# Performance work log

Hardware: AMD Instinct MI355X
Metric: run time of the kernel (lower is better)

## Reference

```python
import jax, jax.numpy as jnp
import numpy as np

COMMITMENT_COST = 0.25

def setup_inputs() -> dict:
    key = jax.random.key(0)
    k1, k2 = jax.random.split(key)
    z = jax.random.normal(k1, (32768, 512), dtype=jnp.float32)
    # codebook initialized uniform(-1/K, 1/K) as in the torch module
    K = 8192
    W = jax.random.uniform(k2, (K, 512), dtype=jnp.float32, minval=-1.0 / K, maxval=1.0 / K)
    return {"z": z, "W": W}

def reference(z, W):
    # z: [B, D], W: [K, D]
    # squared-distance expansion: ||z||^2 + ||w||^2 - 2 z.w
    d2 = (jnp.sum(z * z, axis=1, keepdims=True)
          + jnp.sum(W * W, axis=1)
          - 2.0 * jnp.einsum('bd,kd->bk', z, W))  # [B, K]
    indices = jnp.argmin(d2, axis=1)              # [B]
    z_q_raw = W[indices]                          # [B, D]
    e_latent_loss = jnp.mean((jax.lax.stop_gradient(z_q_raw) - z) ** 2)
    q_latent_loss = jnp.mean((z_q_raw - jax.lax.stop_gradient(z)) ** 2)
    vq_loss = q_latent_loss + COMMITMENT_COST * e_latent_loss
    # straight-through estimator
    z_q = z + jax.lax.stop_gradient(z_q_raw - z)
    return (z_q, indices, vq_loss)
```

## Files before the change

kernel.cpp:

```cpp
#include <hip/hip_runtime.h>
#include <stdint.h>


#define B_ROWS 32768
#define DIM    512
#define KCODES 8192
#define SUPERS 4
#define TILES  16
#define ZROWS  64

typedef short bhalf8_t __attribute__((ext_vector_type(8)));
typedef float f32x4_t  __attribute__((ext_vector_type(4)));

__device__ __forceinline__ float b2f(unsigned short u) {
    return __uint_as_float(((unsigned int)u) << 16);
}
__device__ __forceinline__ unsigned short f2b(float f) {
    unsigned int x = __float_as_uint(f);
    return (unsigned short)((x + 0x7FFFu + ((x >> 16) & 1u)) >> 16);
}
__device__ __forceinline__ void gl_lds16(const void* g, void* l) {
    __builtin_amdgcn_global_load_lds(
        (const __attribute__((address_space(1))) unsigned int*)g,
        (__attribute__((address_space(3))) unsigned int*)l, 16, 0, 0);
}

__global__ __launch_bounds__(256) void k_split(const float4* __restrict__ src,
                                               ushort4* __restrict__ dst, int n4) {
    int i = blockIdx.x * 256 + threadIdx.x;
    int stride = gridDim.x * 256;
    for (; i < n4; i += stride) {
        float4 v = src[i];
        ushort4 h;
        h.x = f2b(v.x); h.y = f2b(v.y); h.z = f2b(v.z); h.w = f2b(v.w);
        dst[i] = h;
    }
}

__global__ __launch_bounds__(256) void k_pairsq(const float* __restrict__ X,
                                                float* __restrict__ out, int nrows) {
    int wid = threadIdx.x >> 6, lane = threadIdx.x & 63;
    int r = blockIdx.x * 4 + wid;
    if (r >= nrows) return;
    int b = lane >> 3, j = lane & 7;
    float acc = 0.f;
    if (b < 4) {
        const float* x = X + (size_t)r * DIM + b * 128 + j;
        float v = x[0];
        acc = __fmul_rn(v, v);
        for (int i = 1; i < 16; i++) {
            float w = x[8 * i];
            acc = __fadd_rn(acc, __fmul_rn(w, w));
        }
    }
    float t = __fadd_rn(acc, __shfl_xor(acc, 1));
    t = __fadd_rn(t, __shfl_xor(t, 2));
    t = __fadd_rn(t, __shfl_xor(t, 4));
    float u = __fadd_rn(t, __shfl_xor(t, 8));
    u = __fadd_rn(u, __shfl_xor(u, 16));
    if (lane == 0) out[r] = u;
}

__global__ __launch_bounds__(256) void k_argmin(const unsigned short* __restrict__ Zh,
                                                const unsigned short* __restrict__ Wh,
                                                const float* __restrict__ ww,
                                                float2* __restrict__ part) {
    __shared__ alignas(16) unsigned char smem[73728];
    const int tid = threadIdx.x;
    const int lane = tid & 63, w = tid >> 6;
    const int wm = w >> 1, wn = w & 1;
    const int lane15 = lane & 15, q = lane >> 4;
    const int b = blockIdx.x;
    const int super = b & 3;
    const int rb = (b >> 2) * ZROWS;

    unsigned char* zl = smem;
    unsigned char* wl = smem + 65536;

    {
        const int m = tid & 15;
        const int kseg8 = ((tid >> 4) & 3) << 3;
#pragma unroll
        for (int i = 0; i < 16; i++) {
            const int s = i * 256 + tid;
            const int ks = s >> 8;
            const int g = (s >> 6) & 3;
            gl_lds16(Zh + (size_t)(rb + g * 16 + m) * DIM + ks * 32 + kseg8,
                     zl + s * 16);
        }
    }

    const int rowO0 = ((tid >> 6) << 4) | (tid & 15);
    const int kO0   = ((tid >> 4) & 3) << 3;
    const int dst0  = tid * 16;

    uint32_t p1[2][4], p2[2][4];
#pragma unroll
    for (int i = 0; i < 2; i++)
#pragma unroll
        for (int jj = 0; jj < 4; jj++) { p1[i][jj] = 0xFFFFFFFFu; p2[i][jj] = 0xFFFFFFFFu; }

    __syncthreads();

    for (int tl = 0; tl < TILES; ++tl) {
        const int nt = super * 2048 + tl * 128;
        f32x4_t acc[2][4];
#pragma unroll
        for (int i = 0; i < 2; i++)
#pragma unroll
            for (int jj = 0; jj < 4; jj++) acc[i][jj] = (f32x4_t){0.f, 0.f, 0.f, 0.f};

        for (int ks = 0; ks < 16; ++ks) {
            __syncthreads();
            const int kg = ks * 32 + kO0;
            gl_lds16(Wh + (size_t)(nt + rowO0) * DIM + kg,      wl + dst0);
            gl_lds16(Wh + (size_t)(nt + rowO0 + 64) * DIM + kg, wl + 4096 + dst0);
            __syncthreads();

            bhalf8_t af[2], bf[4];
#pragma unroll
            for (int f = 0; f < 2; f++)
                af[f] = *(const bhalf8_t*)(zl + ks * 4096 + (wm * 2 + f) * 1024 + lane * 16);
#pragma unroll
            for (int f = 0; f < 4; f++)
                bf[f] = *(const bhalf8_t*)(wl + (wn * 4096 + f * 1024) + lane * 16);
#pragma unroll
            for (int fm = 0; fm < 2; fm++)
#pragma unroll
                for (int fn = 0; fn < 4; fn++)
                    acc[fm][fn] = __builtin_amdgcn_mfma_f32_16x16x32_bf16(af[fm], bf[fn], acc[fm][fn], 0, 0, 0);
        }

        float cb[4];
#pragma unroll
        for (int fn = 0; fn < 4; fn++)
            cb[fn] = ww[nt + wn * 64 + fn * 16 + lane15] + 0.5f;
#pragma unroll
        for (int fm = 0; fm < 2; fm++)
#pragma unroll
            for (int r = 0; r < 4; r++)
#pragma unroll
                for (int fn = 0; fn < 4; fn++) {
                    float sv = fmaf(-2.0f, acc[fm][fn][r], cb[fn]);
                    uint32_t pk = (__float_as_uint(sv) & 0xFFFFFF80u) | (uint32_t)(tl * 4 + fn);
                    if (pk < p1[fm][r]) { p2[fm][r] = p1[fm][r]; p1[fm][r] = pk; }
                    else if (pk < p2[fm][r]) { p2[fm][r] = pk; }
                }
    }

    __syncthreads();
    uint32_t* keys = (uint32_t*)smem;
#pragma unroll
    for (int fm = 0; fm < 2; fm++)
#pragma unroll
        for (int r = 0; r < 4; r++) {
            int row = wm * 32 + fm * 16 + q * 4 + r;
            int slice = wn * 16 + lane15;
            keys[(row * 32 + slice) * 2 + 0] = p1[fm][r];
            keys[(row * 32 + slice) * 2 + 1] = p2[fm][r];
        }
    __syncthreads();
    if (tid < ZROWS) {
        int row = tid;
        int rglob = rb + row;
        for (int s = 0; s < 4; s++) {
            uint32_t bk = 0xFFFFFFFFu; int be = 0;
            for (int e = 0; e < 64; e++) {
                uint32_t k = keys[row * 64 + e];
                if (k < bk) { bk = k; be = e; }
            }
            int slice = be >> 1;
            int id = (int)(bk & 127u);
            int n = super * 2048 + (id >> 2) * 128 + (slice >> 4) * 64 + (id & 3) * 16 + (slice & 15);
            part[((size_t)rglob * SUPERS + super) * 4 + s] =
                make_float2(__uint_as_float(bk), __int_as_float(n));
            keys[row * 64 + be] = 0xFFFFFFFFu;
        }
    }
}

__global__ __launch_bounds__(256) void k_exact(const float* __restrict__ Zf,
                                               const float* __restrict__ Wf,
                                               const float2* __restrict__ part,
                                               const float* __restrict__ zz,
                                               const float* __restrict__ ww,
                                               float* __restrict__ outf,
                                               float* __restrict__ lossp) {
    __shared__ float wsum[4];
    int wid = threadIdx.x >> 6, lane = threadIdx.x & 63;
    int r = blockIdx.x * 4 + wid;
    int c = lane >> 2, j = lane & 3;

    float2 P = part[((size_t)r * SUPERS + (c >> 2)) * 4 + (c & 3)];
    int n = __float_as_int(P.y);
    n = min(max(n, 0), KCODES - 1);

    const float* zp = Zf + (size_t)r * DIM + j;
    const float* wp = Wf + (size_t)n * DIM + j;
    float acc = 0.f;
    for (int i = 0; i < 128; i++)
        acc = __fadd_rn(acc, __fmul_rn(zp[4 * i], wp[4 * i]));
    float t = __fadd_rn(acc, __shfl_xor(acc, 1));
    t = __fadd_rn(t, __shfl_xor(t, 2));
    float dot = __shfl(t, c * 4);

    float t1 = __fadd_rn(zz[r], ww[n]);
    float t2 = __fmul_rn(2.0f, dot);
    float d2 = __fadd_rn(t1, -t2);

    float bd = (j == 0) ? d2 : 3.4e38f;
    int   bn = (j == 0) ? n  : 0x7FFFFFFF;
#pragma unroll
    for (int off = 32; off; off >>= 1) {
        float od = __shfl_xor(bd, off);
        int   on = __shfl_xor(bn, off);
        if (od < bd || (od == bd && on < bn)) { bd = od; bn = on; }
    }
    int idx = bn;

    float4 wa = *(const float4*)(Wf + (size_t)idx * DIM + lane * 8);
    float4 wb = *(const float4*)(Wf + (size_t)idx * DIM + lane * 8 + 4);
    float4 za = *(const float4*)(Zf + (size_t)r   * DIM + lane * 8);
    float4 zb = *(const float4*)(Zf + (size_t)r   * DIM + lane * 8 + 4);
    *(float4*)(outf + (size_t)r * DIM + lane * 8)     = wa;
    *(float4*)(outf + (size_t)r * DIM + lane * 8 + 4) = wb;
    float d0 = za.x - wa.x, d1 = za.y - wa.y, dd2 = za.z - wa.z, d3 = za.w - wa.w;
    float d4 = zb.x - wb.x, d5 = zb.y - wb.y, d6 = zb.z - wb.z, d7 = zb.w - wb.w;
    float ls = d0*d0 + d1*d1 + dd2*dd2 + d3*d3 + d4*d4 + d5*d5 + d6*d6 + d7*d7;
#pragma unroll
    for (int off = 32; off; off >>= 1) ls += __shfl_xor(ls, off);
    if (lane == 0) {
        outf[(size_t)B_ROWS * DIM + r] = (float)idx;
        wsum[wid] = ls;
    }
    __syncthreads();
    if (threadIdx.x == 0) lossp[blockIdx.x] = wsum[0] + wsum[1] + wsum[2] + wsum[3];
}

__global__ __launch_bounds__(256) void k_loss(const float* __restrict__ lossp,
                                              float* __restrict__ outf) {
    __shared__ float sm[256];
    float a = 0.f;
    for (int i = threadIdx.x; i < 8192; i += 256) a += lossp[i];
    sm[threadIdx.x] = a;
    __syncthreads();
    for (int s = 128; s; s >>= 1) {
        if (threadIdx.x < s) sm[threadIdx.x] += sm[threadIdx.x + s];
        __syncthreads();
    }
    if (threadIdx.x == 0)
        outf[(size_t)B_ROWS * DIM + B_ROWS] = 1.25f * sm[0] / 16777216.0f;
}

extern "C" void kernel_launch(void* const* d_in, const int* in_sizes, int n_in,
                              void* d_out, int out_size, void* d_ws, size_t ws_size,
                              hipStream_t stream) {
    (void)in_sizes; (void)n_in; (void)out_size; (void)ws_size;
    const float* Zf = (const float*)d_in[0];
    const float* Wf = (const float*)d_in[1];
    float* outf = (float*)d_out;

    unsigned short* Zh = (unsigned short*)d_out;
    unsigned short* Wh = (unsigned short*)((char*)d_out + (32ull << 20));

    float*  ww    = (float*)d_ws;
    float*  zz    = (float*)((char*)d_ws + 32768);
    float*  lossp = (float*)((char*)d_ws + 163840);
    float2* partp = (float2*)((char*)d_ws + 196608);

    k_split<<<1024, 256, 0, stream>>>((const float4*)Zf, (ushort4*)Zh, B_ROWS * DIM / 4);
    k_split<<<512,  256, 0, stream>>>((const float4*)Wf, (ushort4*)Wh, KCODES * DIM / 4);
    k_pairsq<<<KCODES / 4, 256, 0, stream>>>(Wf, ww, KCODES);
    k_pairsq<<<B_ROWS / 4, 256, 0, stream>>>(Zf, zz, B_ROWS);
    k_argmin<<<(B_ROWS / ZROWS) * SUPERS, 256, 0, stream>>>(Zh, Wh, ww, partp);
    k_exact<<<B_ROWS / 4, 256, 0, stream>>>(Zf, Wf, partp, zz, ww, outf, lossp);
    k_loss<<<1, 256, 0, stream>>>(lossp, outf);
}
```

Baseline: 909.5 us.

## Double-buffer codebook tiles in LDS and pad key array to avoid bank conflicts

The W tile loads into LDS now use two buffers, so the load for the next k-slice is issued while the MFMAs for the current slice run. This halves the barriers per slice and lets global-to-LDS latency overlap with compute across tile boundaries. The top-2 key scratch array is padded to a row stride of 65 to reduce LDS bank conflicts in the per-row scan. LDS use grows to 80KB per block, which may limit occupancy, and the async gl_lds completion relies on the barrier placement being correct.

```diff
diff --git a/kernel.cpp b/kernel.cpp
--- a/kernel.cpp
+++ b/kernel.cpp
@@ -61,11 +61,29 @@
     if (lane == 0) out[r] = u;
 }
 
+__device__ __forceinline__ void compute_slice2(const unsigned char* zl, int ks,
+                                               const unsigned char* wbuf,
+                                               int wm, int wn, int lane,
+                                               f32x4_t acc[2][4]) {
+    bhalf8_t af[2], bf[4];
+#pragma unroll
+    for (int f = 0; f < 2; f++)
+        af[f] = *(const bhalf8_t*)(zl + ks * 4096 + (wm * 2 + f) * 1024 + lane * 16);
+#pragma unroll
+    for (int f = 0; f < 4; f++)
+        bf[f] = *(const bhalf8_t*)(wbuf + wn * 4096 + f * 1024 + lane * 16);
+#pragma unroll
+    for (int fm = 0; fm < 2; fm++)
+#pragma unroll
+        for (int fn = 0; fn < 4; fn++)
+            acc[fm][fn] = __builtin_amdgcn_mfma_f32_16x16x32_bf16(af[fm], bf[fn], acc[fm][fn], 0, 0, 0);
+}
+
 __global__ __launch_bounds__(256) void k_argmin(const unsigned short* __restrict__ Zh,
                                                 const unsigned short* __restrict__ Wh,
                                                 const float* __restrict__ ww,
                                                 float2* __restrict__ part) {
-    __shared__ alignas(16) unsigned char smem[73728];
+    __shared__ alignas(16) unsigned char smem[81920];
     const int tid = threadIdx.x;
     const int lane = tid & 63, w = tid >> 6;
     const int wm = w >> 1, wn = w & 1;
@@ -74,8 +92,9 @@
     const int super = b & 3;
     const int rb = (b >> 2) * ZROWS;
 
-    unsigned char* zl = smem;
-    unsigned char* wl = smem + 65536;
+    unsigned char* zl  = smem;
+    unsigned char* wl0 = smem + 65536;
+    unsigned char* wl1 = smem + 65536 + 8192;
 
     {
         const int m = tid & 15;
@@ -94,47 +113,50 @@
     const int kO0   = ((tid >> 4) & 3) << 3;
     const int dst0  = tid * 16;
 
+#define STAGE_W(ST, WB)                                                          \
+    do {                                                                         \
+        const int _tl = (ST) >> 4;                                               \
+        const int _nt = super * 2048 + _tl * 128;                                \
+        const int _kg = ((ST) & 15) * 32 + kO0;                                  \
+        gl_lds16(Wh + (size_t)(_nt + rowO0) * DIM + _kg,      (WB) + dst0);      \
+        gl_lds16(Wh + (size_t)(_nt + rowO0 + 64) * DIM + _kg, (WB) + 4096 + dst0);\
+    } while (0)
+
     uint32_t p1[2][4], p2[2][4];
 #pragma unroll
     for (int i = 0; i < 2; i++)
 #pragma unroll
         for (int jj = 0; jj < 4; jj++) { p1[i][jj] = 0xFFFFFFFFu; p2[i][jj] = 0xFFFFFFFFu; }
 
+    STAGE_W(0, wl0);
     __syncthreads();
 
     for (int tl = 0; tl < TILES; ++tl) {
         const int nt = super * 2048 + tl * 128;
-        f32x4_t acc[2][4];
-#pragma unroll
-        for (int i = 0; i < 2; i++)
-#pragma unroll
-            for (int jj = 0; jj < 4; jj++) acc[i][jj] = (f32x4_t){0.f, 0.f, 0.f, 0.f};
-
-        for (int ks = 0; ks < 16; ++ks) {
-            __syncthreads();
-            const int kg = ks * 32 + kO0;
-            gl_lds16(Wh + (size_t)(nt + rowO0) * DIM + kg,      wl + dst0);
-            gl_lds16(Wh + (size_t)(nt + rowO0 + 64) * DIM + kg, wl + 4096 + dst0);
-            __syncthreads();
-
-            bhalf8_t af[2], bf[4];
-#pragma unroll
-            for (int f = 0; f < 2; f++)
-                af[f] = *(const bhalf8_t*)(zl + ks * 4096 + (wm * 2 + f) * 1024 + lane * 16);
-#pragma unroll
-            for (int f = 0; f < 4; f++)
-                bf[f] = *(const bhalf8_t*)(wl + (wn * 4096 + f * 1024) + lane * 16);
-#pragma unroll
-            for (int fm = 0; fm < 2; fm++)
-#pragma unroll
-                for (int fn = 0; fn < 4; fn++)
-                    acc[fm][fn] = __builtin_amdgcn_mfma_f32_16x16x32_bf16(af[fm], bf[fn], acc[fm][fn], 0, 0, 0);
-        }
 
         float cb[4];
 #pragma unroll
         for (int fn = 0; fn < 4; fn++)
             cb[fn] = ww[nt + wn * 64 + fn * 16 + lane15] + 0.5f;
+
+        f32x4_t acc[2][4];
+#pragma unroll
+        for (int i = 0; i < 2; i++)
+#pragma unroll
+            for (int jj = 0; jj < 4; jj++) acc[i][jj] = (f32x4_t){0.f, 0.f, 0.f, 0.f};
+
+        for (int k2 = 0; k2 < 16; k2 += 2) {
+            const int st = tl * 16 + k2;
+            STAGE_W(st + 1, wl1);
+            compute_slice2(zl, k2, wl0, wm, wn, lane, acc);
+            __syncthreads();
+            if (st + 2 < SUPERS * 0 + TILES * 16) {
+                STAGE_W(st + 2, wl0);
+            }
+            compute_slice2(zl, k2 + 1, wl1, wm, wn, lane, acc);
+            __syncthreads();
+        }
+
 #pragma unroll
         for (int fm = 0; fm < 2; fm++)
 #pragma unroll
@@ -147,6 +169,7 @@
                     else if (pk < p2[fm][r]) { p2[fm][r] = pk; }
                 }
     }
+#undef STAGE_W
 
     __syncthreads();
     uint32_t* keys = (uint32_t*)smem;
@@ -156,8 +179,8 @@
         for (int r = 0; r < 4; r++) {
             int row = wm * 32 + fm * 16 + q * 4 + r;
             int slice = wn * 16 + lane15;
-            keys[(row * 32 + slice) * 2 + 0] = p1[fm][r];
-            keys[(row * 32 + slice) * 2 + 1] = p2[fm][r];
+            keys[row * 65 + slice * 2 + 0] = p1[fm][r];
+            keys[row * 65 + slice * 2 + 1] = p2[fm][r];
         }
     __syncthreads();
     if (tid < ZROWS) {
@@ -166,7 +189,7 @@
         for (int s = 0; s < 4; s++) {
             uint32_t bk = 0xFFFFFFFFu; int be = 0;
             for (int e = 0; e < 64; e++) {
-                uint32_t k = keys[row * 64 + e];
+                uint32_t k = keys[row * 65 + e];
                 if (k < bk) { bk = k; be = e; }
             }
             int slice = be >> 1;
@@ -174,7 +197,7 @@
             int n = super * 2048 + (id >> 2) * 128 + (slice >> 4) * 64 + (id & 3) * 16 + (slice & 15);
             part[((size_t)rglob * SUPERS + super) * 4 + s] =
                 make_float2(__uint_as_float(bk), __int_as_float(n));
-            keys[row * 64 + be] = 0xFFFFFFFFu;
+            keys[row * 65 + be] = 0xFFFFFFFFu;
         }
     }
 }
```

After: 844.9 us. -7.1%, faster.

## Give each wave private double-buffered W tiles and drop per-step block barriers

Applied to the files above, without the earlier changes.

Each wave now stages its own 32-column slice of the codebook into a private, double-buffered LDS region and uses vmcnt waits instead of two block-wide __syncthreads per k-step. The wave tiling changes from 2x2 (32 rows x 64 codes) to 1x4 (all 64 rows x 32 codes), so every wave reads all Z fragments from LDS. The top-2 candidate merge is widened to 128 keys per row with padded stride. The aim is to overlap global-to-LDS loads with MFMA and remove barrier stalls, at the cost of more LDS and more Z fragment reads per wave.

```diff
diff --git a/kernel.cpp b/kernel.cpp
--- a/kernel.cpp
+++ b/kernel.cpp
@@ -8,6 +8,7 @@
 #define SUPERS 4
 #define TILES  16
 #define ZROWS  64
+#define NSTEP  256
 
 typedef short bhalf8_t __attribute__((ext_vector_type(8)));
 typedef float f32x4_t  __attribute__((ext_vector_type(4)));
@@ -61,21 +62,37 @@
     if (lane == 0) out[r] = u;
 }
 
+__device__ __forceinline__ void compute_ks(const unsigned char* zl, int ks,
+                                           const unsigned char* wbuf,
+                                           int lane, f32x4_t acc[4][2]) {
+    bhalf8_t af[4], bf[2];
+#pragma unroll
+    for (int f = 0; f < 4; f++)
+        af[f] = *(const bhalf8_t*)(zl + ks * 4096 + f * 1024 + lane * 16);
+#pragma unroll
+    for (int f = 0; f < 2; f++)
+        bf[f] = *(const bhalf8_t*)(wbuf + f * 1024 + lane * 16);
+#pragma unroll
+    for (int fm = 0; fm < 4; fm++)
+#pragma unroll
+        for (int fn = 0; fn < 2; fn++)
+            acc[fm][fn] = __builtin_amdgcn_mfma_f32_16x16x32_bf16(af[fm], bf[fn], acc[fm][fn], 0, 0, 0);
+}
+
 __global__ __launch_bounds__(256) void k_argmin(const unsigned short* __restrict__ Zh,
                                                 const unsigned short* __restrict__ Wh,
                                                 const float* __restrict__ ww,
                                                 float2* __restrict__ part) {
-    __shared__ alignas(16) unsigned char smem[73728];
+    __shared__ alignas(16) unsigned char smem[81920];
     const int tid = threadIdx.x;
     const int lane = tid & 63, w = tid >> 6;
-    const int wm = w >> 1, wn = w & 1;
     const int lane15 = lane & 15, q = lane >> 4;
     const int b = blockIdx.x;
     const int super = b & 3;
     const int rb = (b >> 2) * ZROWS;
 
-    unsigned char* zl = smem;
-    unsigned char* wl = smem + 65536;
+    unsigned char* zl  = smem;
+    unsigned char* wpr = smem + 65536 + w * 4096;
 
     {
         const int m = tid & 15;
@@ -90,74 +107,75 @@
         }
     }
 
-    const int rowO0 = ((tid >> 6) << 4) | (tid & 15);
-    const int kO0   = ((tid >> 4) & 3) << 3;
-    const int dst0  = tid * 16;
-
-    uint32_t p1[2][4], p2[2][4];
-#pragma unroll
-    for (int i = 0; i < 2; i++)
+    const int colL = lane & 15;
+    const int ksegL8 = (q & 3) << 3;
+#define STAGE_W(ST, WB)                                                                   \
+    do {                                                                                  \
+        const int _nt = super * 2048 + ((ST) >> 4) * 128 + w * 32;                        \
+        const int _kg = ((ST) & 15) * 32 + ksegL8;                                        \
+        gl_lds16(Wh + (size_t)(_nt + colL) * DIM + _kg,      (WB) + lane * 16);           \
+        gl_lds16(Wh + (size_t)(_nt + 16 + colL) * DIM + _kg, (WB) + 1024 + lane * 16);    \
+    } while (0)
+
+    uint32_t p1[4][4], p2[4][4];
+#pragma unroll
+    for (int i = 0; i < 4; i++)
 #pragma unroll
         for (int jj = 0; jj < 4; jj++) { p1[i][jj] = 0xFFFFFFFFu; p2[i][jj] = 0xFFFFFFFFu; }
 
+    STAGE_W(0, wpr);
     __syncthreads();
 
     for (int tl = 0; tl < TILES; ++tl) {
         const int nt = super * 2048 + tl * 128;
-        f32x4_t acc[2][4];
-#pragma unroll
-        for (int i = 0; i < 2; i++)
-#pragma unroll
-            for (int jj = 0; jj < 4; jj++) acc[i][jj] = (f32x4_t){0.f, 0.f, 0.f, 0.f};
-
-        for (int ks = 0; ks < 16; ++ks) {
-            __syncthreads();
-            const int kg = ks * 32 + kO0;
-            gl_lds16(Wh + (size_t)(nt + rowO0) * DIM + kg,      wl + dst0);
-            gl_lds16(Wh + (size_t)(nt + rowO0 + 64) * DIM + kg, wl + 4096 + dst0);
-            __syncthreads();
-
-            bhalf8_t af[2], bf[4];
-#pragma unroll
-            for (int f = 0; f < 2; f++)
-                af[f] = *(const bhalf8_t*)(zl + ks * 4096 + (wm * 2 + f) * 1024 + lane * 16);
-#pragma unroll
-            for (int f = 0; f < 4; f++)
-                bf[f] = *(const bhalf8_t*)(wl + (wn * 4096 + f * 1024) + lane * 16);
-#pragma unroll
-            for (int fm = 0; fm < 2; fm++)
-#pragma unroll
-                for (int fn = 0; fn < 4; fn++)
-                    acc[fm][fn] = __builtin_amdgcn_mfma_f32_16x16x32_bf16(af[fm], bf[fn], acc[fm][fn], 0, 0, 0);
-        }
-
-        float cb[4];
-#pragma unroll
-        for (int fn = 0; fn < 4; fn++)
-            cb[fn] = ww[nt + wn * 64 + fn * 16 + lane15] + 0.5f;
-#pragma unroll
-        for (int fm = 0; fm < 2; fm++)
+        float cb[2];
+        cb[0] = ww[nt + w * 32 + lane15] + 0.5f;
+        cb[1] = ww[nt + w * 32 + 16 + lane15] + 0.5f;
+
+        f32x4_t acc[4][2];
+#pragma unroll
+        for (int i = 0; i < 4; i++)
+#pragma unroll
+            for (int jj = 0; jj < 2; jj++) acc[i][jj] = (f32x4_t){0.f, 0.f, 0.f, 0.f};
+
+        for (int k2 = 0; k2 < 16; k2 += 2) {
+            const int st = tl * 16 + k2;
+            STAGE_W(st + 1, wpr + 2048);
+            asm volatile("s_waitcnt vmcnt(2)" ::: "memory");
+            compute_ks(zl, k2, wpr, lane, acc);
+            if (st + 2 < NSTEP) {
+                STAGE_W(st + 2, wpr);
+                asm volatile("s_waitcnt vmcnt(2)" ::: "memory");
+            } else {
+                asm volatile("s_waitcnt vmcnt(0)" ::: "memory");
+            }
+            compute_ks(zl, k2 + 1, wpr + 2048, lane, acc);
+        }
+
+#pragma unroll
+        for (int fm = 0; fm < 4; fm++)
 #pragma unroll
             for (int r = 0; r < 4; r++)
 #pragma unroll
-                for (int fn = 0; fn < 4; fn++) {
+                for (int fn = 0; fn < 2; fn++) {
                     float sv = fmaf(-2.0f, acc[fm][fn][r], cb[fn]);
-                    uint32_t pk = (__float_as_uint(sv) & 0xFFFFFF80u) | (uint32_t)(tl * 4 + fn);
+                    uint32_t pk = (__float_as_uint(sv) & 0xFFFFFF80u) | (uint32_t)(tl * 2 + fn);
                     if (pk < p1[fm][r]) { p2[fm][r] = p1[fm][r]; p1[fm][r] = pk; }
                     else if (pk < p2[fm][r]) { p2[fm][r] = pk; }
                 }
     }
+#undef STAGE_W
 
     __syncthreads();
     uint32_t* keys = (uint32_t*)smem;
 #pragma unroll
-    for (int fm = 0; fm < 2; fm++)
+    for (int fm = 0; fm < 4; fm++)
 #pragma unroll
         for (int r = 0; r < 4; r++) {
-            int row = wm * 32 + fm * 16 + q * 4 + r;
-            int slice = wn * 16 + lane15;
-            keys[(row * 32 + slice) * 2 + 0] = p1[fm][r];
-            keys[(row * 32 + slice) * 2 + 1] = p2[fm][r];
+            int row = fm * 16 + q * 4 + r;
+            int sp = w * 16 + lane15;
+            keys[row * 130 + sp * 2 + 0] = p1[fm][r];
+            keys[row * 130 + sp * 2 + 1] = p2[fm][r];
         }
     __syncthreads();
     if (tid < ZROWS) {
@@ -165,16 +183,16 @@
         int rglob = rb + row;
         for (int s = 0; s < 4; s++) {
             uint32_t bk = 0xFFFFFFFFu; int be = 0;
-            for (int e = 0; e < 64; e++) {
-                uint32_t k = keys[row * 64 + e];
+            for (int e = 0; e < 128; e++) {
+                uint32_t k = keys[row * 130 + e];
                 if (k < bk) { bk = k; be = e; }
             }
-            int slice = be >> 1;
+            int sp = be >> 1;
             int id = (int)(bk & 127u);
-            int n = super * 2048 + (id >> 2) * 128 + (slice >> 4) * 64 + (id & 3) * 16 + (slice & 15);
+            int n = super * 2048 + (id >> 1) * 128 + (sp >> 4) * 32 + (id & 1) * 16 + (sp & 15);
             part[((size_t)rglob * SUPERS + super) * 4 + s] =
                 make_float2(__uint_as_float(bk), __int_as_float(n));
-            keys[row * 64 + be] = 0xFFFFFFFFu;
+            keys[row * 130 + be] = 0xFFFFFFFFu;
         }
     }
 }
```

Measured after the change: 793.3 us. 1.15x faster.
